# Performance work log

Measured on AMD Instinct MI355X. Metric: run time of the kernel, lower is better.

Reference implementation:

```python
import jax, jax.numpy as jnp
import numpy as np

B, T = 64, 2048
RNN_DIM, EMB_DIM, ATTN_DIM = 1024, 512, 128
N_FILT, KSIZE = 32, 31
PAD = (KSIZE - 1) // 2


def setup_inputs() -> dict:
    key = jax.random.key(0)
    ks = jax.random.split(key, 8)
    s = 0.02
    return {
        "attention_hidden_state": jax.random.normal(ks[0], (B, RNN_DIM), jnp.float32),
        "memory": jax.random.normal(ks[1], (B, T, EMB_DIM), jnp.float32),
        "processed_memory": jax.random.normal(ks[2], (B, T, ATTN_DIM), jnp.float32),
        "attention_weights_cat": jax.random.uniform(ks[3], (B, 2, T), jnp.float32),
        "mask": jnp.zeros((B, T), dtype=bool),
        "Wq": jax.random.normal(ks[4], (ATTN_DIM, RNN_DIM), jnp.float32) * s,
        "Wconv": jax.random.normal(ks[5], (N_FILT, 2, KSIZE), jnp.float32) * s,
        "Wloc": jax.random.normal(ks[6], (ATTN_DIM, N_FILT), jnp.float32) * s,
        "Wv": jax.random.normal(ks[7], (1, ATTN_DIM), jnp.float32) * s,
    }


def reference(attention_hidden_state, memory, processed_memory,
              attention_weights_cat, mask, Wq, Wconv, Wloc, Wv):
    # query projection: [B, rnn] -> [B, 1, attn]
    pq = jnp.einsum("br,ar->ba", attention_hidden_state, Wq)[:, None, :]
    # location conv: [B, 2, T] -> [B, F, T]
    conv = jax.lax.conv_general_dilated(
        attention_weights_cat, Wconv, window_strides=(1,),
        padding=[(PAD, PAD)], dimension_numbers=("NCH", "OIH", "NCH"))
    # [B, T, F] @ Wloc.T -> [B, T, attn]
    ploc = jnp.einsum("bft,af->bta", conv, Wloc)
    # energies: [B, T]
    energies = jnp.einsum("bta,oa->bto", jnp.tanh(pq + ploc + processed_memory), Wv)[..., 0]
    alignment = jnp.where(mask, -jnp.inf, energies)
    attention_weights = jax.nn.softmax(alignment, axis=1)
    # context: [B, emb]
    attention_context = jnp.einsum("bt,bte->be", attention_weights, memory)
    return attention_context, attention_weights
```

## Files before the change

### kernel.cpp

```cpp
#include <hip/hip_runtime.h>
#include <math.h>

#define BB 64
#define TT 2048
#define RNN 1024
#define EMB 512
#define ATTN 128
#define NF 32
#define KS 31
#define PADW 15

#define TIL 32
#define CHT 8
#define NCH (TT / CHT)

__device__ __forceinline__ float fast_tanh(float x) {
    float ax = fabsf(x);
    float e = __expf(-2.f * ax);
    float r = (1.f - e) * __builtin_amdgcn_rcpf(1.f + e);
    return copysignf(r, x);
}

__global__ __launch_bounds__(256) void pq_kernel(const float* __restrict__ h,
                                                 const float* __restrict__ Wq,
                                                 float* __restrict__ pq) {
    int b = blockIdx.x >> 2;
    int q = blockIdx.x & 3;
    __shared__ float s_h[RNN];
    for (int i = threadIdx.x; i < RNN; i += 256) s_h[i] = h[b * RNN + i];
    __syncthreads();

    int wave = threadIdx.x >> 6;
    int lane = threadIdx.x & 63;
#pragma unroll 2
    for (int j = 0; j < 8; ++j) {
        int a = q * 32 + wave * 8 + j;
        const float4* wq4 = (const float4*)(Wq + (size_t)a * RNN);
        float acc = 0.f;
#pragma unroll
        for (int i = 0; i < 4; ++i) {
            float4 w4 = wq4[lane + 64 * i];
            float4 h4 = *(const float4*)(s_h + 4 * (lane + 64 * i));
            acc += w4.x * h4.x + w4.y * h4.y + w4.z * h4.z + w4.w * h4.w;
        }
#pragma unroll
        for (int off = 32; off > 0; off >>= 1) acc += __shfl_xor(acc, off, 64);
        if (lane == 0) pq[b * ATTN + a] = acc;
    }
}

__global__ __launch_bounds__(256) void fused3_kernel(
    const float* __restrict__ pm,
    const float* __restrict__ awc,
    const float* __restrict__ mem,
    const unsigned char* __restrict__ mask,
    const float* __restrict__ pq,
    const float* __restrict__ Wconv,
    const float* __restrict__ Wloc,
    const float* __restrict__ Wv,
    float* __restrict__ wp,
    float* __restrict__ ms,
    float* __restrict__ cp)
{
    int b = blockIdx.x >> 6;
    int blk = blockIdx.x & 63;
    int t0 = blk * TIL;
    int tid = threadIdx.x;
    int w = tid >> 6;
    int l = tid & 63;

    __shared__ __align__(16) float s_ploc[TIL][ATTN];
    __shared__ __align__(16) float s_conv[TIL][40];
    __shared__ float s_awc[2][TIL + 2 * PADW + 2];
    __shared__ float s_pq[ATTN];
    __shared__ float s_wv[ATTN];

    for (int i = tid; i < 2 * (TIL + 2 * PADW); i += 256) {
        int c = i / (TIL + 2 * PADW);
        int j = i % (TIL + 2 * PADW);
        int tg = t0 - PADW + j;
        s_awc[c][j] = (tg >= 0 && tg < TT) ? awc[((size_t)b * 2 + c) * TT + tg] : 0.f;
    }
    if (tid < ATTN) {
        s_pq[tid] = pq[b * ATTN + tid];
        s_wv[tid] = Wv[tid];
    }
    __syncthreads();

    {
        int t = tid & 31;
        int fq = tid >> 5;
        float a0 = 0.f, a1 = 0.f, a2 = 0.f, a3 = 0.f;
#pragma unroll
        for (int c = 0; c < 2; ++c) {
            const float* wc = Wconv + (size_t)((fq * 4) * 2 + c) * KS;
#pragma unroll
            for (int k = 0; k < KS; ++k) {
                float av = s_awc[c][t + k];
                a0 += av * wc[k];
                a1 += av * wc[2 * KS + k];
                a2 += av * wc[4 * KS + k];
                a3 += av * wc[6 * KS + k];
            }
        }
        s_conv[t][fq * 4 + 0] = a0;
        s_conv[t][fq * 4 + 1] = a1;
        s_conv[t][fq * 4 + 2] = a2;
        s_conv[t][fq * 4 + 3] = a3;
    }
    __syncthreads();

    {
        int a = tid & 127;
        int tg = tid >> 7;
        const float4* wlr = (const float4*)(Wloc + (size_t)a * NF);
        float4 w0 = wlr[0], w1 = wlr[1], w2 = wlr[2], w3 = wlr[3];
        float4 w4 = wlr[4], w5 = wlr[5], w6 = wlr[6], w7 = wlr[7];
#pragma unroll
        for (int tt = 0; tt < 16; ++tt) {
            int t = tg * 16 + tt;
            const float4* cv = (const float4*)&s_conv[t][0];
            float4 c0 = cv[0], c1 = cv[1], c2 = cv[2], c3 = cv[3];
            float4 c4 = cv[4], c5 = cv[5], c6 = cv[6], c7 = cv[7];
            float acc;
            acc  = c0.x * w0.x + c0.y * w0.y + c0.z * w0.z + c0.w * w0.w;
            acc += c1.x * w1.x + c1.y * w1.y + c1.z * w1.z + c1.w * w1.w;
            acc += c2.x * w2.x + c2.y * w2.y + c2.z * w2.z + c2.w * w2.w;
            acc += c3.x * w3.x + c3.y * w3.y + c3.z * w3.z + c3.w * w3.w;
            acc += c4.x * w4.x + c4.y * w4.y + c4.z * w4.z + c4.w * w4.w;
            acc += c5.x * w5.x + c5.y * w5.y + c5.z * w5.z + c5.w * w5.w;
            acc += c6.x * w6.x + c6.y * w6.y + c6.z * w6.z + c6.w * w6.w;
            acc += c7.x * w7.x + c7.y * w7.y + c7.z * w7.z + c7.w * w7.w;
            s_ploc[t][a] = acc;
        }
    }
    __syncthreads();

    float pq0 = s_pq[l], pq1 = s_pq[l + 64];
    float wv0 = s_wv[l], wv1 = s_wv[l + 64];

    float pA[CHT], pB[CHT];
#pragma unroll
    for (int i = 0; i < CHT; ++i) {
        const float* r = pm + ((size_t)b * TT + t0 + w * CHT + i) * ATTN;
        pA[i] = r[l];
        pB[i] = r[l + 64];
    }
    float e[CHT];
#pragma unroll
    for (int i = 0; i < CHT; ++i) {
        int t = w * CHT + i;
        float v0 = pq0 + pA[i] + s_ploc[t][l];
        float v1 = pq1 + pB[i] + s_ploc[t][l + 64];
        e[i] = wv0 * fast_tanh(v0) + wv1 * fast_tanh(v1);
    }
#pragma unroll
    for (int off = 32; off > 0; off >>= 1)
#pragma unroll
        for (int i = 0; i < CHT; ++i) e[i] += __shfl_xor(e[i], off, 64);

    {
        const unsigned int* mk = (const unsigned int*)(mask + (size_t)b * TT + t0 + w * CHT);
        unsigned int m0 = mk[0], m1 = mk[1];
#pragma unroll
        for (int j = 0; j < 4; ++j) {
            if ((m0 >> (8 * j)) & 0xff) e[j] = -1e30f;
            if ((m1 >> (8 * j)) & 0xff) e[4 + j] = -1e30f;
        }
    }

    float m = e[0];
#pragma unroll
    for (int i = 1; i < CHT; ++i) m = fmaxf(m, e[i]);
    float p[CHT], s = 0.f;
#pragma unroll
    for (int i = 0; i < CHT; ++i) {
        p[i] = __expf(e[i] - m);
        s += p[i];
    }
    int ch = blk * 4 + w;
    if (l == 0) {
        ms[((size_t)b * NCH + ch) * 2 + 0] = m;
        ms[((size_t)b * NCH + ch) * 2 + 1] = s;
    }
    {
        float pv = p[0];
#pragma unroll
        for (int i = 1; i < CHT; ++i)
            if (l == i) pv = p[i];
        if (l < CHT) wp[(size_t)b * TT + t0 + w * CHT + l] = pv;
    }

    float4 A0 = {0.f, 0.f, 0.f, 0.f}, A1 = {0.f, 0.f, 0.f, 0.f};
    const float4* m4 = (const float4*)(mem + ((size_t)b * TT + t0 + w * CHT) * EMB);
#pragma unroll
    for (int i = 0; i < CHT; ++i) {
        float pv = p[i];
        float4 v0 = m4[(size_t)i * (EMB / 4) + l];
        float4 v1 = m4[(size_t)i * (EMB / 4) + 64 + l];
        A0.x += pv * v0.x; A0.y += pv * v0.y; A0.z += pv * v0.z; A0.w += pv * v0.w;
        A1.x += pv * v1.x; A1.y += pv * v1.y; A1.z += pv * v1.z; A1.w += pv * v1.w;
    }
    float4* cp4 = (float4*)(cp + ((size_t)b * NCH + ch) * EMB);
    cp4[l] = A0;
    cp4[64 + l] = A1;
}

__global__ __launch_bounds__(256) void combine_kernel(
    const float* __restrict__ wp, const float* __restrict__ ms,
    const float* __restrict__ cp, float* __restrict__ ctx,
    float* __restrict__ wts) {
    int b = blockIdx.x;
    int tid = threadIdx.x;
    __shared__ float s_m[NCH], s_s[NCH], s_scale[NCH];
    if (tid < NCH) {
        s_m[tid] = ms[((size_t)b * NCH + tid) * 2 + 0];
        s_s[tid] = ms[((size_t)b * NCH + tid) * 2 + 1];
    }
    __syncthreads();
    float M = -1e30f;
#pragma unroll 8
    for (int c = 0; c < NCH; ++c) M = fmaxf(M, s_m[c]);
    float S = 0.f;
#pragma unroll 8
    for (int c = 0; c < NCH; ++c) S += s_s[c] * __expf(s_m[c] - M);
    float invS = 1.f / S;
    if (tid < NCH) s_scale[tid] = __expf(s_m[tid] - M) * invS;
    __syncthreads();

    {
        float2 acc = {0.f, 0.f};
        const float2* cp2 = (const float2*)(cp + (size_t)b * NCH * EMB);
#pragma unroll 8
        for (int c = 0; c < NCH; ++c) {
            float sc = s_scale[c];
            float2 v = cp2[(size_t)c * (EMB / 2) + tid];
            acc.x += sc * v.x;
            acc.y += sc * v.y;
        }
        ((float2*)(ctx + (size_t)b * EMB))[tid] = acc;
    }
#pragma unroll
    for (int i = 0; i < 8; ++i) {
        int t = i * 256 + tid;
        wts[(size_t)b * TT + t] = wp[(size_t)b * TT + t] * s_scale[t >> 3];
    }
}

extern "C" void kernel_launch(void* const* d_in, const int* in_sizes, int n_in,
                              void* d_out, int out_size, void* d_ws, size_t ws_size,
                              hipStream_t stream) {
    const float* h    = (const float*)d_in[0];
    const float* mem  = (const float*)d_in[1];
    const float* pmem = (const float*)d_in[2];
    const float* awc  = (const float*)d_in[3];
    const unsigned char* mask = (const unsigned char*)d_in[4];
    const float* Wq   = (const float*)d_in[5];
    const float* Wcv  = (const float*)d_in[6];
    const float* Wloc = (const float*)d_in[7];
    const float* Wv   = (const float*)d_in[8];

    float* out = (float*)d_out;
    float* ctx = out;
    float* wts = out + BB * EMB;

    float* ws = (float*)d_ws;
    float* pq = ws;
    float* wp = pq + BB * ATTN;
    float* ms = wp + BB * TT;
    float* cp = ms + BB * NCH * 2;

    pq_kernel<<<BB * 4, 256, 0, stream>>>(h, Wq, pq);
    fused3_kernel<<<BB * 64, 256, 0, stream>>>(pmem, awc, mem, mask, pq, Wcv,
                                               Wloc, Wv, wp, ms, cp);
    combine_kernel<<<BB, 256, 0, stream>>>(wp, ms, cp, ctx, wts);
}
```

Before: 131.6 us.

## Split context reduction out of energy kernel into separate partial/reduce passes

```diff
diff --git a/kernel.cpp b/kernel.cpp
--- a/kernel.cpp
+++ b/kernel.cpp
@@ -14,6 +14,10 @@
 #define CHT 8
 #define NCH (TT / CHT)
 
+#define SEG_T 64
+#define NSEG (TT / SEG_T)
+#define NPART (NSEG * 2)
+
 __device__ __forceinline__ float fast_tanh(float x) {
     float ax = fabsf(x);
     float e = __expf(-2.f * ax);
@@ -49,18 +53,16 @@
     }
 }
 
-__global__ __launch_bounds__(256) void fused3_kernel(
+__global__ __launch_bounds__(256) void energy_kernel(
     const float* __restrict__ pm,
     const float* __restrict__ awc,
-    const float* __restrict__ mem,
     const unsigned char* __restrict__ mask,
     const float* __restrict__ pq,
     const float* __restrict__ Wconv,
     const float* __restrict__ Wloc,
     const float* __restrict__ Wv,
     float* __restrict__ wp,
-    float* __restrict__ ms,
-    float* __restrict__ cp)
+    float* __restrict__ ms)
 {
     int b = blockIdx.x >> 6;
     int blk = blockIdx.x & 63;
@@ -72,18 +74,12 @@
     __shared__ __align__(16) float s_ploc[TIL][ATTN];
     __shared__ __align__(16) float s_conv[TIL][40];
     __shared__ float s_awc[2][TIL + 2 * PADW + 2];
-    __shared__ float s_pq[ATTN];
-    __shared__ float s_wv[ATTN];
 
     for (int i = tid; i < 2 * (TIL + 2 * PADW); i += 256) {
         int c = i / (TIL + 2 * PADW);
         int j = i % (TIL + 2 * PADW);
         int tg = t0 - PADW + j;
         s_awc[c][j] = (tg >= 0 && tg < TT) ? awc[((size_t)b * 2 + c) * TT + tg] : 0.f;
-    }
-    if (tid < ATTN) {
-        s_pq[tid] = pq[b * ATTN + tid];
-        s_wv[tid] = Wv[tid];
     }
     __syncthreads();
 
@@ -136,23 +132,22 @@
     }
     __syncthreads();
 
-    float pq0 = s_pq[l], pq1 = s_pq[l + 64];
-    float wv0 = s_wv[l], wv1 = s_wv[l + 64];
-
-    float pA[CHT], pB[CHT];
-#pragma unroll
-    for (int i = 0; i < CHT; ++i) {
-        const float* r = pm + ((size_t)b * TT + t0 + w * CHT + i) * ATTN;
-        pA[i] = r[l];
-        pB[i] = r[l + 64];
-    }
+    float2 pq2 = *(const float2*)(pq + b * ATTN + 2 * l);
+    float2 wv2 = *(const float2*)(Wv + 2 * l);
+
+    float2 pAB[CHT];
+#pragma unroll
+    for (int i = 0; i < CHT; ++i)
+        pAB[i] = *(const float2*)(pm + ((size_t)b * TT + t0 + w * CHT + i) * ATTN + 2 * l);
+
     float e[CHT];
 #pragma unroll
     for (int i = 0; i < CHT; ++i) {
         int t = w * CHT + i;
-        float v0 = pq0 + pA[i] + s_ploc[t][l];
-        float v1 = pq1 + pB[i] + s_ploc[t][l + 64];
-        e[i] = wv0 * fast_tanh(v0) + wv1 * fast_tanh(v1);
+        float2 pl2 = *(const float2*)&s_ploc[t][2 * l];
+        float v0 = pq2.x + pAB[i].x + pl2.x;
+        float v1 = pq2.y + pAB[i].y + pl2.y;
+        e[i] = wv2.x * fast_tanh(v0) + wv2.y * fast_tanh(v1);
     }
 #pragma unroll
     for (int off = 32; off > 0; off >>= 1)
@@ -190,33 +185,16 @@
             if (l == i) pv = p[i];
         if (l < CHT) wp[(size_t)b * TT + t0 + w * CHT + l] = pv;
     }
-
-    float4 A0 = {0.f, 0.f, 0.f, 0.f}, A1 = {0.f, 0.f, 0.f, 0.f};
-    const float4* m4 = (const float4*)(mem + ((size_t)b * TT + t0 + w * CHT) * EMB);
-#pragma unroll
-    for (int i = 0; i < CHT; ++i) {
-        float pv = p[i];
-        float4 v0 = m4[(size_t)i * (EMB / 4) + l];
-        float4 v1 = m4[(size_t)i * (EMB / 4) + 64 + l];
-        A0.x += pv * v0.x; A0.y += pv * v0.y; A0.z += pv * v0.z; A0.w += pv * v0.w;
-        A1.x += pv * v1.x; A1.y += pv * v1.y; A1.z += pv * v1.z; A1.w += pv * v1.w;
-    }
-    float4* cp4 = (float4*)(cp + ((size_t)b * NCH + ch) * EMB);
-    cp4[l] = A0;
-    cp4[64 + l] = A1;
-}
-
-__global__ __launch_bounds__(256) void combine_kernel(
+}
+
+__global__ __launch_bounds__(256) void scales_kernel(
     const float* __restrict__ wp, const float* __restrict__ ms,
-    const float* __restrict__ cp, float* __restrict__ ctx,
     float* __restrict__ wts) {
     int b = blockIdx.x;
     int tid = threadIdx.x;
     __shared__ float s_m[NCH], s_s[NCH], s_scale[NCH];
-    if (tid < NCH) {
-        s_m[tid] = ms[((size_t)b * NCH + tid) * 2 + 0];
-        s_s[tid] = ms[((size_t)b * NCH + tid) * 2 + 1];
-    }
+    s_m[tid] = ms[((size_t)b * NCH + tid) * 2 + 0];
+    s_s[tid] = ms[((size_t)b * NCH + tid) * 2 + 1];
     __syncthreads();
     float M = -1e30f;
 #pragma unroll 8
@@ -225,26 +203,53 @@
 #pragma unroll 8
     for (int c = 0; c < NCH; ++c) S += s_s[c] * __expf(s_m[c] - M);
     float invS = 1.f / S;
-    if (tid < NCH) s_scale[tid] = __expf(s_m[tid] - M) * invS;
-    __syncthreads();
-
-    {
-        float2 acc = {0.f, 0.f};
-        const float2* cp2 = (const float2*)(cp + (size_t)b * NCH * EMB);
-#pragma unroll 8
-        for (int c = 0; c < NCH; ++c) {
-            float sc = s_scale[c];
-            float2 v = cp2[(size_t)c * (EMB / 2) + tid];
-            acc.x += sc * v.x;
-            acc.y += sc * v.y;
-        }
-        ((float2*)(ctx + (size_t)b * EMB))[tid] = acc;
-    }
+    s_scale[tid] = __expf(s_m[tid] - M) * invS;
+    __syncthreads();
 #pragma unroll
     for (int i = 0; i < 8; ++i) {
         int t = i * 256 + tid;
         wts[(size_t)b * TT + t] = wp[(size_t)b * TT + t] * s_scale[t >> 3];
     }
+}
+
+__global__ __launch_bounds__(256) void ctx_partial_kernel(
+    const float* __restrict__ mem,
+    const float* __restrict__ wts,
+    float* __restrict__ partial)
+{
+    int b = blockIdx.x >> 5;
+    int seg = blockIdx.x & 31;
+    int tid = threadIdx.x;
+    int e4 = tid & 127;
+    int half = tid >> 7;
+
+    __shared__ float s_w[SEG_T];
+    if (tid < SEG_T) s_w[tid] = wts[(size_t)b * TT + seg * SEG_T + tid];
+    __syncthreads();
+
+    float4 acc = {0.f, 0.f, 0.f, 0.f};
+    const float4* m4 = (const float4*)(mem + ((size_t)b * TT + seg * SEG_T) * EMB) +
+                       (size_t)half * (EMB / 4) + e4;
+#pragma unroll 8
+    for (int i = 0; i < SEG_T / 2; ++i) {
+        float wv = s_w[2 * i + half];
+        float4 mv = m4[(size_t)i * (2 * EMB / 4)];
+        acc.x += wv * mv.x;
+        acc.y += wv * mv.y;
+        acc.z += wv * mv.z;
+        acc.w += wv * mv.w;
+    }
+    float4* p4 = (float4*)(partial + ((size_t)(seg * 2 + half) * BB + b) * EMB) + e4;
+    *p4 = acc;
+}
+
+__global__ __launch_bounds__(256) void ctx_reduce_kernel(
+    const float* __restrict__ partial, float* __restrict__ ctx) {
+    int idx = blockIdx.x * 256 + threadIdx.x;
+    float acc = 0.f;
+#pragma unroll 8
+    for (int s = 0; s < NPART; ++s) acc += partial[(size_t)s * (BB * EMB) + idx];
+    ctx[idx] = acc;
 }
 
 extern "C" void kernel_launch(void* const* d_in, const int* in_sizes, int n_in,
@@ -268,10 +273,12 @@
     float* pq = ws;
     float* wp = pq + BB * ATTN;
     float* ms = wp + BB * TT;
-    float* cp = ms + BB * NCH * 2;
+    float* partial = ms + BB * NCH * 2;
 
     pq_kernel<<<BB * 4, 256, 0, stream>>>(h, Wq, pq);
-    fused3_kernel<<<BB * 64, 256, 0, stream>>>(pmem, awc, mem, mask, pq, Wcv,
-                                               Wloc, Wv, wp, ms, cp);
-    combine_kernel<<<BB, 256, 0, stream>>>(wp, ms, cp, ctx, wts);
-}
+    energy_kernel<<<BB * 64, 256, 0, stream>>>(pmem, awc, mask, pq, Wcv, Wloc,
+                                               Wv, wp, ms);
+    scales_kernel<<<BB, 256, 0, stream>>>(wp, ms, wts);
+    ctx_partial_kernel<<<BB * NSEG, 256, 0, stream>>>(mem, wts, partial);
+    ctx_reduce_kernel<<<(BB * EMB) / 256, 256, 0, stream>>>(partial, ctx);
+}
```

Result: slower. 140.0 us (+6.4%).
